# Kernel tuning notes

Measured on AMD Instinct MI355X. Metric: run time of the kernel, lower is better.

Reference implementation:

```python
import jax, jax.numpy as jnp
import numpy as np
import math

N_HEAD = 8
D_MODEL = 512
HEAD_SIZE = D_MODEL // N_HEAD
VOCAB = 16384
BLOCK = 512
LN_EPS = 1e-5


def sinusoidal_pe(max_len, dim):
    pos = np.arange(max_len)[:, None].astype(np.float32)
    div = np.exp(np.arange(0, dim, 2).astype(np.float32) * (-math.log(10000.0) / dim))
    pe = np.zeros((max_len, dim), dtype=np.float32)
    pe[:, 0::2] = np.sin(pos * div)
    pe[:, 1::2] = np.cos(pos * div)
    return jnp.asarray(pe)  # (max_len, hs)


def setup_inputs() -> dict:
    key = jax.random.key(0)
    ks = jax.random.split(key, 6)
    b, t = 4, BLOCK
    return {
        "x": jax.random.normal(ks[0], (b, t, 1), dtype=jnp.float32),
        "embedding": jax.random.normal(ks[1], (N_HEAD, VOCAB, HEAD_SIZE), dtype=jnp.float32),
        "enc_w": jax.random.normal(ks[2], (D_MODEL, 1), dtype=jnp.float32) * 0.05,
        "enc_b": jax.random.normal(ks[3], (D_MODEL,), dtype=jnp.float32) * 0.05,
        "ln_w": jnp.ones((HEAD_SIZE,), dtype=jnp.float32),
        "ln_b": jnp.zeros((HEAD_SIZE,), dtype=jnp.float32),
        "dec_w": jax.random.normal(ks[4], (1, D_MODEL), dtype=jnp.float32) * 0.05,
        "dec_b": jax.random.normal(ks[5], (1,), dtype=jnp.float32) * 0.05,
    }


def reference(x, embedding, enc_w, enc_b, ln_w, ln_b, dec_w, dec_b):
    b, t, _ = x.shape
    # encoder: Linear(input_dim -> d_model)
    h = x @ enc_w.T + enc_b                              # (b, t, d_model)
    h = h.reshape(b, t, N_HEAD, HEAD_SIZE).transpose(0, 2, 1, 3)  # (b, nh, t, hs)
    # sinusoidal positional encoding over time, added to head dim
    h = h + sinusoidal_pe(BLOCK, HEAD_SIZE)[:t]
    # LayerNorm over hs
    mu = h.mean(-1, keepdims=True)
    var = ((h - mu) ** 2).mean(-1, keepdims=True)
    h = (h - mu) * jax.lax.rsqrt(var + LN_EPS) * ln_w + ln_b
    # attention over shared per-head codebook
    scores = jnp.einsum('bnth,nvh->bntv', h, embedding) / math.sqrt(D_MODEL)
    probs = jax.nn.softmax(scores, axis=-1)              # (b, nh, t, vocab)
    quant = jnp.einsum('bntv,nvh->bnth', probs, embedding)
    quant = quant.transpose(0, 2, 1, 3).reshape(b, t, D_MODEL)
    # decoder: Linear(d_model -> output_dim)
    return quant @ dec_w.T + dec_b                       # (b, t, 1)
```

## Files before the change

### kernel.cpp

```cpp
#include <hip/hip_runtime.h>
#include <hip/hip_bf16.h>
#include <math.h>

#define NH 8
#define HS 64
#define VOCAB 16384
#define QPH 2048
#define NSLICE 32
#define QSCALE (0.04419417382415922f * 1.4426950408889634f)

typedef __attribute__((ext_vector_type(8))) short bf16x8;
typedef __attribute__((ext_vector_type(4))) float f32x4;

static __device__ __forceinline__ unsigned short f2bf(float f) {
    __hip_bfloat16 h = __float2bfloat16(f);
    unsigned short u;
    __builtin_memcpy(&u, &h, 2);
    return u;
}

static __device__ __forceinline__ float fexp2(float x) {
#if __has_builtin(__builtin_amdgcn_exp2f)
    return __builtin_amdgcn_exp2f(x);
#else
    return __expf(x * 0.6931471805599453f);
#endif
}

static __device__ __forceinline__ void stage16(const void* g, void* l) {
    __builtin_amdgcn_global_load_lds(
        (const __attribute__((address_space(1))) void*)g,
        (__attribute__((address_space(3))) void*)l, 16, 0, 0);
}

__global__ void eprep(const float* __restrict__ emb, const float* __restrict__ dec_w,
                      unsigned short* __restrict__ ebf, float* __restrict__ g) {
    int i4  = blockIdx.x * 256 + threadIdx.x;
    int row = i4 >> 4;
    int c4  = i4 & 15;
    int n   = row >> 14;
    int v   = row & (VOCAB - 1);
    f32x4 vv = ((const f32x4*)emb)[i4];
    ushort4 u = make_ushort4(f2bf(vv.x), f2bf(vv.y), f2bf(vv.z), f2bf(vv.w));
    int T = v >> 4, r = v & 15;
    int h = c4 >> 3, q = (c4 >> 1) & 3, jh = c4 & 1;
    size_t o4 = ((((size_t)(n * 1024 + T) * 2 + h) * 4 + q) * 16 + r) * 2 + jh;
    ((ushort4*)ebf)[o4] = u;
    const float* dw = dec_w + n * 64 + c4 * 4;
    float p = vv.x * dw[0] + vv.y * dw[1] + vv.z * dw[2] + vv.w * dw[3];
    p += __shfl_xor(p, 1); p += __shfl_xor(p, 2);
    p += __shfl_xor(p, 4); p += __shfl_xor(p, 8);
    if (c4 == 0) g[row] = p;
}

__global__ void qprep(const float* __restrict__ x, const float* __restrict__ enc_w,
                      const float* __restrict__ enc_b, const float* __restrict__ ln_w,
                      const float* __restrict__ ln_b, unsigned short* __restrict__ qbf) {
    int row  = blockIdx.x * 4 + (threadIdx.x >> 6);
    int h    = threadIdx.x & 63;
    int n = row >> 11;
    int q = row & 2047;
    int t = q & 511;
    float xv = x[q];
    int d = n * 64 + h;
    float h2  = (float)(h & ~1);
    float div = __expf(h2 * (-9.210340371976184f / 64.0f));
    float ang = (float)t * div;
    float pe  = (h & 1) ? __cosf(ang) : __sinf(ang);
    float v = xv * enc_w[d] + enc_b[d] + pe;
    float s = v;
    #pragma unroll
    for (int off = 1; off < 64; off <<= 1) s += __shfl_xor(s, off);
    float mu = s * (1.0f / 64.0f);
    float dd = v - mu;
    float s2 = dd * dd;
    #pragma unroll
    for (int off = 1; off < 64; off <<= 1) s2 += __shfl_xor(s2, off);
    float var = s2 * (1.0f / 64.0f);
    float y = dd * rsqrtf(var + 1e-5f) * ln_w[h] + ln_b[h];
    qbf[row * 64 + h] = f2bf(y * QSCALE);
}

__global__ void __launch_bounds__(256, 4)
attn(const unsigned short* __restrict__ qbf, const unsigned short* __restrict__ ebf,
     const float* __restrict__ g, float2* __restrict__ part) {
    __shared__ __attribute__((aligned(16))) char smem[2 * 4096 + 2048];
    float* gl = (float*)(smem + 8192);

    int tid  = threadIdx.x;
    int w    = tid >> 6;
    int lane = tid & 63;
    int quad = lane >> 4;
    int l15  = lane & 15;
    int head   = blockIdx.x & 7;
    int vslice = (blockIdx.x >> 3) & 31;
    int qchunk = blockIdx.x >> 8;
    int qbase  = (qchunk * 4 + w) * 128;

    const char* esrc = (const char*)ebf + (size_t)(head * 1024 + vslice * 32) * 2048;
    const float* gp  = g + head * VOCAB + vslice * 512;

    stage16(esrc + tid * 16, smem + w * 1024);
    ((float2*)gl)[tid] = ((const float2*)gp)[tid];

    const short* qp = (const short*)qbf + (size_t)(head * QPH + qbase) * HS;
    bf16x8 qf[8][2];
    #pragma unroll
    for (int qt = 0; qt < 8; ++qt) {
        const short* qrow = qp + (qt * 16 + l15) * HS + quad * 8;
        qf[qt][0] = *(const bf16x8*)(qrow);
        qf[qt][1] = *(const bf16x8*)(qrow + 32);
    }

    float num[8] = {0.f, 0.f, 0.f, 0.f, 0.f, 0.f, 0.f, 0.f};
    float den[8] = {0.f, 0.f, 0.f, 0.f, 0.f, 0.f, 0.f, 0.f};
    const f32x4 z = {0.f, 0.f, 0.f, 0.f};

    __syncthreads();

    #pragma clang loop unroll(disable)
    for (int it = 0; it < 16; ++it) {
        if (it < 15)
            stage16(esrc + (it + 1) * 4096 + tid * 16,
                    smem + ((it + 1) & 1) * 4096 + w * 1024);

        const char* abase = smem + (it & 1) * 4096 + lane * 16;
        bf16x8 a00 = *(const bf16x8*)(abase);
        bf16x8 a01 = *(const bf16x8*)(abase + 1024);
        bf16x8 a10 = *(const bf16x8*)(abase + 2048);
        bf16x8 a11 = *(const bf16x8*)(abase + 3072);
        f32x4 gv0 = *(const f32x4*)(gl + it * 32 + quad * 4);
        f32x4 gv1 = *(const f32x4*)(gl + it * 32 + 16 + quad * 4);

        #pragma unroll
        for (int qt = 0; qt < 8; ++qt) {
            f32x4 acc0 = __builtin_amdgcn_mfma_f32_16x16x32_bf16(a00, qf[qt][0], z, 0, 0, 0);
            acc0       = __builtin_amdgcn_mfma_f32_16x16x32_bf16(a01, qf[qt][1], acc0, 0, 0, 0);
            f32x4 acc1 = __builtin_amdgcn_mfma_f32_16x16x32_bf16(a10, qf[qt][0], z, 0, 0, 0);
            acc1       = __builtin_amdgcn_mfma_f32_16x16x32_bf16(a11, qf[qt][1], acc1, 0, 0, 0);
            #pragma unroll
            for (int r = 0; r < 4; ++r) {
                float p0 = fexp2(acc0[r]);
                float p1 = fexp2(acc1[r]);
                den[qt] += p0 + p1;
                num[qt] += p0 * gv0[r] + p1 * gv1[r];
            }
        }
        __syncthreads();
    }

    #pragma unroll
    for (int qt = 0; qt < 8; ++qt) {
        num[qt] += __shfl_xor(num[qt], 16); num[qt] += __shfl_xor(num[qt], 32);
        den[qt] += __shfl_xor(den[qt], 16); den[qt] += __shfl_xor(den[qt], 32);
    }
    #pragma unroll
    for (int j = 0; j < 2; ++j) {
        int qt = quad * 2 + j;
        int qg = qbase + qt * 16 + l15;
        part[((size_t)vslice * NH + head) * QPH + qg] = make_float2(num[qt], den[qt]);
    }
}

__global__ void fin(const float2* __restrict__ part, const float* __restrict__ dec_b,
                    float* __restrict__ out) {
    __shared__ float red[8][32];
    int t  = threadIdx.x;
    int ql = t & 31;
    int n  = t >> 5;
    int q  = blockIdx.x * 32 + ql;
    float nv = 0.f, dv = 0.f;
    #pragma unroll 8
    for (int sl = 0; sl < NSLICE; ++sl) {
        float2 nd = part[((size_t)sl * NH + n) * QPH + q];
        nv += nd.x; dv += nd.y;
    }
    red[n][ql] = nv / dv;
    __syncthreads();
    if (t < 32) {
        float s = dec_b[0];
        #pragma unroll
        for (int m = 0; m < NH; ++m) s += red[m][t];
        out[q] = s;
    }
}

extern "C" void kernel_launch(void* const* d_in, const int* in_sizes, int n_in,
                              void* d_out, int out_size, void* d_ws, size_t ws_size,
                              hipStream_t stream) {
    const float* x     = (const float*)d_in[0];
    const float* emb   = (const float*)d_in[1];
    const float* enc_w = (const float*)d_in[2];
    const float* enc_b = (const float*)d_in[3];
    const float* ln_w  = (const float*)d_in[4];
    const float* ln_b  = (const float*)d_in[5];
    const float* dec_w = (const float*)d_in[6];
    const float* dec_b = (const float*)d_in[7];
    float* out = (float*)d_out;

    char* ws = (char*)d_ws;
    unsigned short* qbf  = (unsigned short*)(ws);
    unsigned short* ebf  = (unsigned short*)(ws + 2097152);
    float*          g    = (float*)(ws + 2097152 + 16777216);
    float2*         part = (float2*)(ws + 2097152 + 16777216 + 524288);

    hipLaunchKernelGGL(eprep, dim3(8192), dim3(256), 0, stream, emb, dec_w, ebf, g);
    hipLaunchKernelGGL(qprep, dim3(4096), dim3(256), 0, stream, x, enc_w, enc_b, ln_w, ln_b, qbf);
    hipLaunchKernelGGL(attn,  dim3(1024), dim3(256), 0, stream, qbf, ebf, g, part);
    hipLaunchKernelGGL(fin,   dim3(64),   dim3(256), 0, stream, part, dec_b, out);
}
```

Before: 155.2 us.

## Stage queries in LDS and stream embedding tiles per wave from global

The attention kernel changes role: each block now holds a 128-query tile of one head in LDS, and each wave walks its own 512-entry vocab slice, loading embedding fragments straight from global into registers without LDS double buffering or per-iteration barriers. qprep writes queries in an MFMA-fragment layout and eprep is rewritten so each block writes one contiguous 16-row tile, reducing the decoder dot product through shared memory. This removes the per-iteration __syncthreads and the LDS staging of the codebook, at the cost of direct global loads in the inner loop and more LDS per block, which may lower occupancy.

```diff
diff --git a/kernel.cpp b/kernel.cpp
--- a/kernel.cpp
+++ b/kernel.cpp
@@ -35,22 +35,31 @@
 
 __global__ void eprep(const float* __restrict__ emb, const float* __restrict__ dec_w,
                       unsigned short* __restrict__ ebf, float* __restrict__ g) {
-    int i4  = blockIdx.x * 256 + threadIdx.x;
-    int row = i4 >> 4;
-    int c4  = i4 & 15;
-    int n   = row >> 14;
-    int v   = row & (VOCAB - 1);
-    f32x4 vv = ((const f32x4*)emb)[i4];
+    __shared__ float red[256];
+    int tid = threadIdx.x;
+    int nt  = blockIdx.x;
+    int h   = (tid >> 7) & 1;
+    int q   = (tid >> 5) & 3;
+    int r   = (tid >> 1) & 15;
+    int jh  = tid & 1;
+    int n   = nt >> 10;
+    int T   = nt & 1023;
+    int row = n * VOCAB + T * 16 + r;
+    int c4  = h * 8 + q * 2 + jh;
+    f32x4 vv = ((const f32x4*)emb)[(size_t)row * 16 + c4];
     ushort4 u = make_ushort4(f2bf(vv.x), f2bf(vv.y), f2bf(vv.z), f2bf(vv.w));
-    int T = v >> 4, r = v & 15;
-    int h = c4 >> 3, q = (c4 >> 1) & 3, jh = c4 & 1;
-    size_t o4 = ((((size_t)(n * 1024 + T) * 2 + h) * 4 + q) * 16 + r) * 2 + jh;
-    ((ushort4*)ebf)[o4] = u;
+    ((ushort4*)ebf)[(size_t)nt * 256 + tid] = u;
     const float* dw = dec_w + n * 64 + c4 * 4;
     float p = vv.x * dw[0] + vv.y * dw[1] + vv.z * dw[2] + vv.w * dw[3];
-    p += __shfl_xor(p, 1); p += __shfl_xor(p, 2);
-    p += __shfl_xor(p, 4); p += __shfl_xor(p, 8);
-    if (c4 == 0) g[row] = p;
+    red[tid] = p;
+    __syncthreads();
+    if (tid < 16) {
+        float s = 0.f;
+        #pragma unroll
+        for (int m = 0; m < 16; ++m)
+            s += red[((m >> 3) * 128) + (((m & 7) >> 1) * 32) + tid * 2 + (m & 1)];
+        g[n * VOCAB + T * 16 + tid] = s;
+    }
 }
 
 __global__ void qprep(const float* __restrict__ x, const float* __restrict__ enc_w,
@@ -78,14 +87,21 @@
     for (int off = 1; off < 64; off <<= 1) s2 += __shfl_xor(s2, off);
     float var = s2 * (1.0f / 64.0f);
     float y = dd * rsqrtf(var + 1e-5f) * ln_w[h] + ln_b[h];
-    qbf[row * 64 + h] = f2bf(y * QSCALE);
+    int qt   = (q >> 4) & 7;
+    int l15  = q & 15;
+    int kf   = h >> 5;
+    int quad = (h >> 3) & 3;
+    int j    = h & 7;
+    size_t idx = ((size_t)(n * 16 + (q >> 7)) * 8192)
+               + ((size_t)((qt * 2 + kf) * 4 + quad) * 128) + l15 * 8 + j;
+    qbf[idx] = f2bf(y * QSCALE);
 }
 
 __global__ void __launch_bounds__(256, 4)
 attn(const unsigned short* __restrict__ qbf, const unsigned short* __restrict__ ebf,
      const float* __restrict__ g, float2* __restrict__ part) {
-    __shared__ __attribute__((aligned(16))) char smem[2 * 4096 + 2048];
-    float* gl = (float*)(smem + 8192);
+    __shared__ __attribute__((aligned(16))) char smem[16384 + 8192];
+    float* gl = (float*)(smem + 16384);
 
     int tid  = threadIdx.x;
     int w    = tid >> 6;
@@ -93,60 +109,58 @@
     int quad = lane >> 4;
     int l15  = lane & 15;
     int head   = blockIdx.x & 7;
-    int vslice = (blockIdx.x >> 3) & 31;
-    int qchunk = blockIdx.x >> 8;
-    int qbase  = (qchunk * 4 + w) * 128;
-
-    const char* esrc = (const char*)ebf + (size_t)(head * 1024 + vslice * 32) * 2048;
-    const float* gp  = g + head * VOCAB + vslice * 512;
-
-    stage16(esrc + tid * 16, smem + w * 1024);
-    ((float2*)gl)[tid] = ((const float2*)gp)[tid];
-
-    const short* qp = (const short*)qbf + (size_t)(head * QPH + qbase) * HS;
-    bf16x8 qf[8][2];
-    #pragma unroll
-    for (int qt = 0; qt < 8; ++qt) {
-        const short* qrow = qp + (qt * 16 + l15) * HS + quad * 8;
-        qf[qt][0] = *(const bf16x8*)(qrow);
-        qf[qt][1] = *(const bf16x8*)(qrow + 32);
-    }
+    int qgroup = (blockIdx.x >> 3) & 15;
+    int vgroup = blockIdx.x >> 7;
+    int vslice = vgroup * 4 + w;
+
+    const char*  qsrc = (const char*)qbf + (size_t)(head * 16 + qgroup) * 16384;
+    const char*  esrc = (const char*)ebf + (size_t)head * 2097152 + (size_t)vslice * 65536;
+    const float* gp   = g + head * VOCAB + vgroup * 2048;
+
+    #pragma unroll
+    for (int k = 0; k < 4; ++k)
+        stage16(qsrc + k * 4096 + tid * 16, smem + k * 4096 + w * 1024);
+    stage16((const char*)gp + tid * 16,        (char*)gl + w * 1024);
+    stage16((const char*)gp + 4096 + tid * 16, (char*)gl + 4096 + w * 1024);
+    __syncthreads();
 
     float num[8] = {0.f, 0.f, 0.f, 0.f, 0.f, 0.f, 0.f, 0.f};
     float den[8] = {0.f, 0.f, 0.f, 0.f, 0.f, 0.f, 0.f, 0.f};
     const f32x4 z = {0.f, 0.f, 0.f, 0.f};
-
-    __syncthreads();
+    const float* gw = gl + w * 512;
 
     #pragma clang loop unroll(disable)
-    for (int it = 0; it < 16; ++it) {
-        if (it < 15)
-            stage16(esrc + (it + 1) * 4096 + tid * 16,
-                    smem + ((it + 1) & 1) * 4096 + w * 1024);
-
-        const char* abase = smem + (it & 1) * 4096 + lane * 16;
-        bf16x8 a00 = *(const bf16x8*)(abase);
-        bf16x8 a01 = *(const bf16x8*)(abase + 1024);
-        bf16x8 a10 = *(const bf16x8*)(abase + 2048);
-        bf16x8 a11 = *(const bf16x8*)(abase + 3072);
-        f32x4 gv0 = *(const f32x4*)(gl + it * 32 + quad * 4);
-        f32x4 gv1 = *(const f32x4*)(gl + it * 32 + 16 + quad * 4);
+    for (int it = 0; it < 8; ++it) {
+        asm volatile("" ::: "memory");
+        const char* eb = esrc + it * 8192;
+        bf16x8 a[4][2];
+        #pragma unroll
+        for (int vt = 0; vt < 4; ++vt) {
+            a[vt][0] = *(const bf16x8*)(eb + vt * 2048 +        lane * 16);
+            a[vt][1] = *(const bf16x8*)(eb + vt * 2048 + 1024 + lane * 16);
+        }
+        f32x4 gv[4];
+        #pragma unroll
+        for (int vt = 0; vt < 4; ++vt)
+            gv[vt] = *(const f32x4*)(gw + it * 64 + vt * 16 + quad * 4);
 
         #pragma unroll
         for (int qt = 0; qt < 8; ++qt) {
-            f32x4 acc0 = __builtin_amdgcn_mfma_f32_16x16x32_bf16(a00, qf[qt][0], z, 0, 0, 0);
-            acc0       = __builtin_amdgcn_mfma_f32_16x16x32_bf16(a01, qf[qt][1], acc0, 0, 0, 0);
-            f32x4 acc1 = __builtin_amdgcn_mfma_f32_16x16x32_bf16(a10, qf[qt][0], z, 0, 0, 0);
-            acc1       = __builtin_amdgcn_mfma_f32_16x16x32_bf16(a11, qf[qt][1], acc1, 0, 0, 0);
+            const char* qb = smem + qt * 2048 + lane * 16;
+            bf16x8 q0 = *(const bf16x8*)(qb);
+            bf16x8 q1 = *(const bf16x8*)(qb + 1024);
             #pragma unroll
-            for (int r = 0; r < 4; ++r) {
-                float p0 = fexp2(acc0[r]);
-                float p1 = fexp2(acc1[r]);
-                den[qt] += p0 + p1;
-                num[qt] += p0 * gv0[r] + p1 * gv1[r];
+            for (int vt = 0; vt < 4; ++vt) {
+                f32x4 acc = __builtin_amdgcn_mfma_f32_16x16x32_bf16(a[vt][0], q0, z, 0, 0, 0);
+                acc       = __builtin_amdgcn_mfma_f32_16x16x32_bf16(a[vt][1], q1, acc, 0, 0, 0);
+                #pragma unroll
+                for (int r = 0; r < 4; ++r) {
+                    float p = fexp2(acc[r]);
+                    den[qt] += p;
+                    num[qt] += p * gv[vt][r];
+                }
             }
         }
-        __syncthreads();
     }
 
     #pragma unroll
@@ -157,7 +171,7 @@
     #pragma unroll
     for (int j = 0; j < 2; ++j) {
         int qt = quad * 2 + j;
-        int qg = qbase + qt * 16 + l15;
+        int qg = qgroup * 128 + qt * 16 + l15;
         part[((size_t)vslice * NH + head) * QPH + qg] = make_float2(num[qt], den[qt]);
     }
 }
```

New measurement: 141.1 us. 1.1x faster.
